# Kernel optimization log

Hardware: AMD Instinct MI355X
Metric: run time of the kernel (lower is better)

The kernel has to match this reference:

```python
import jax, jax.numpy as jnp
import numpy as np

N = 2000
E = 128
H = 8
DH = E // H
K = 32  # max_neighbors
CLAMP = 1e4


def _sanitize(t):
    t = jnp.nan_to_num(t, nan=0.0, posinf=CLAMP, neginf=-CLAMP)
    return jnp.clip(t, -CLAMP, CLAMP)


def _layernorm(h, g, b, eps=1e-5):
    mu = h.mean(-1, keepdims=True)
    var = ((h - mu) ** 2).mean(-1, keepdims=True)
    return (h - mu) * jax.lax.rsqrt(var + eps) * g + b


def setup_inputs() -> dict:
    key = jax.random.key(0)
    ks = jax.random.split(key, 8)
    x = jax.random.normal(ks[0], (N, E), dtype=jnp.float32)
    coords9 = jax.random.normal(ks[1], (N, 9), dtype=jnp.float32)
    prompt_signal = jax.random.normal(ks[2], (E,), dtype=jnp.float32)
    pe_w = jax.random.normal(ks[3], (3, 32), dtype=jnp.float32) / np.sqrt(3.0)
    pe_b = jnp.zeros((32,), jnp.float32)
    pe_g = jnp.ones((32,), jnp.float32)
    pe_bt = jnp.zeros((32,), jnp.float32)
    in_w = jax.random.normal(ks[4], (3 * E, E), dtype=jnp.float32) / np.sqrt(E)
    in_b = jnp.zeros((3 * E,), jnp.float32)
    out_w = jax.random.normal(ks[5], (E, E), dtype=jnp.float32) / np.sqrt(E)
    out_b = jnp.zeros((E,), jnp.float32)
    return {"x": x, "coords9": coords9, "prompt_signal": prompt_signal,
            "pe_w": pe_w, "pe_b": pe_b, "pe_g": pe_g, "pe_bt": pe_bt,
            "in_w": in_w, "in_b": in_b, "out_w": out_w, "out_b": out_b}


def reference(x, coords9, prompt_signal, pe_w, pe_b, pe_g, pe_bt, in_w, in_b, out_w, out_b):
    n = x.shape[0]
    verts = coords9.reshape(n, 3, 3)
    cent = verts.mean(axis=1)  # (N,3)

    # pairwise centroid distances (only geo-relation channel that affects the output;
    # cos_angles/area_ratios/boundary_sharing feed geo_bias which is dead code in forward)
    diff = cent[:, None, :] - cent[None, :, :]
    dist = jnp.sqrt(jnp.sum(diff * diff, axis=-1) + 1e-20)  # (N,N)

    # positional encoder: Linear(3,32) -> GELU(exact) -> LayerNorm(32)
    pe = jax.nn.gelu(cent @ pe_w + pe_b, approximate=False)
    pe = _layernorm(pe, pe_g, pe_bt)  # (N,32)

    prompt_enhanced = x + prompt_signal[None, :]
    pos_enhanced = jnp.concatenate([prompt_enhanced[:, : 3 * E // 4], pe], axis=-1)  # (N,128)

    # top-K nearest neighbors -> additive attention mask (0 for kept, -inf-like otherwise)
    _, topk_idx = jax.lax.top_k(-dist, K)  # (N,K) smallest distances
    big_neg = jnp.float32(-1e9)
    attn_mask = jnp.full((n, n), big_neg, dtype=jnp.float32)
    attn_mask = attn_mask.at[jnp.arange(n)[:, None], topk_idx].set(0.0)

    # nn.MultiheadAttention (self-attention, eval mode -> no dropout)
    qkv = pos_enhanced @ in_w.T + in_b  # (N,3E)
    q, k, v = jnp.split(qkv, 3, axis=-1)
    q = q.reshape(n, H, DH).transpose(1, 0, 2)  # (H,N,DH)
    k = k.reshape(n, H, DH).transpose(1, 0, 2)
    v = v.reshape(n, H, DH).transpose(1, 0, 2)
    scores = jnp.einsum('hnd,hmd->hnm', q, k) / np.sqrt(DH) + attn_mask[None]
    probs = jax.nn.softmax(scores, axis=-1)
    o = jnp.einsum('hnm,hmd->hnd', probs, v)  # (H,N,DH)
    o = o.transpose(1, 0, 2).reshape(n, E)
    out = o @ out_w.T + out_b
    return _sanitize(out)
```

## Files before the change

### kernel.cpp

```cpp
#include <hip/hip_runtime.h>
#include <math.h>

#define N_NODES 2000
#define E_DIM   128
#define QKV_W   384

__global__ __launch_bounds__(256) void prep_kernel(
    const float* __restrict__ x, const float* __restrict__ coords9,
    const float* __restrict__ ps, const float* __restrict__ pe_w,
    const float* __restrict__ pe_b, const float* __restrict__ pe_g,
    const float* __restrict__ pe_bt,
    float* __restrict__ cent, float* __restrict__ pos)
{
    int tid = threadIdx.x;
    int g = tid >> 5, lane = tid & 31;
    int row = blockIdx.x * 8 + g;

    const float* c9 = coords9 + row * 9;
    float cx = (c9[0] + c9[3] + c9[6]) * (1.0f / 3.0f);
    float cy = (c9[1] + c9[4] + c9[7]) * (1.0f / 3.0f);
    float cz = (c9[2] + c9[5] + c9[8]) * (1.0f / 3.0f);
    if (lane < 3) cent[row * 3 + lane] = (lane == 0) ? cx : ((lane == 1) ? cy : cz);

    #pragma unroll
    for (int k = 0; k < 3; ++k) {
        int c = lane + 32 * k;
        pos[row * E_DIM + c] = x[row * E_DIM + c] + ps[c];
    }

    int j = lane;
    float h = cx * pe_w[j] + cy * pe_w[32 + j] + cz * pe_w[64 + j] + pe_b[j];
    float ge = 0.5f * h * (1.0f + erff(h * 0.7071067811865476f));
    float s = ge;
    #pragma unroll
    for (int m = 16; m >= 1; m >>= 1) s += __shfl_xor(s, m);
    float mu = s * (1.0f / 32.0f);
    float d = ge - mu;
    float v = d * d;
    #pragma unroll
    for (int m = 16; m >= 1; m >>= 1) v += __shfl_xor(v, m);
    float var = v * (1.0f / 32.0f);
    float y = d * (1.0f / sqrtf(var + 1e-5f)) * pe_g[j] + pe_bt[j];
    pos[row * E_DIM + 96 + j] = y;
}

__global__ __launch_bounds__(256) void qkv_kernel(
    const float* __restrict__ pos, const float* __restrict__ in_w,
    const float* __restrict__ in_b, float* __restrict__ qkv)
{
    __shared__ __align__(16) float As[128 * 32];
    int tid = threadIdx.x;
    int rt = blockIdx.x / 3, ct = blockIdx.x % 3;
    int rbase = rt * 32, cbase = ct * 128;

    {
        int r = tid & 31, e0 = (tid >> 5) * 16;
        int row = rbase + r;
        #pragma unroll
        for (int q = 0; q < 4; ++q) {
            int e = e0 + q * 4;
            float4 vv = (row < N_NODES) ? *(const float4*)&pos[row * E_DIM + e]
                                        : make_float4(0.f, 0.f, 0.f, 0.f);
            As[(e + 0) * 32 + r] = vv.x;
            As[(e + 1) * 32 + r] = vv.y;
            As[(e + 2) * 32 + r] = vv.z;
            As[(e + 3) * 32 + r] = vv.w;
        }
    }
    __syncthreads();

    int cg = tid & 31, rg = tid >> 5;
    int c0 = cbase + cg * 4, r0 = rg * 4;
    float acc[4][4];
    #pragma unroll
    for (int i = 0; i < 4; ++i)
        #pragma unroll
        for (int jj = 0; jj < 4; ++jj) acc[i][jj] = 0.f;

    for (int k0 = 0; k0 < 128; k0 += 4) {
        float4 a0 = *(const float4*)&As[(k0 + 0) * 32 + r0];
        float4 a1 = *(const float4*)&As[(k0 + 1) * 32 + r0];
        float4 a2 = *(const float4*)&As[(k0 + 2) * 32 + r0];
        float4 a3 = *(const float4*)&As[(k0 + 3) * 32 + r0];
        #pragma unroll
        for (int ci = 0; ci < 4; ++ci) {
            float4 b = *(const float4*)&in_w[(c0 + ci) * E_DIM + k0];
            acc[0][ci] += a0.x * b.x + a1.x * b.y + a2.x * b.z + a3.x * b.w;
            acc[1][ci] += a0.y * b.x + a1.y * b.y + a2.y * b.z + a3.y * b.w;
            acc[2][ci] += a0.z * b.x + a1.z * b.y + a2.z * b.z + a3.z * b.w;
            acc[3][ci] += a0.w * b.x + a1.w * b.y + a2.w * b.z + a3.w * b.w;
        }
    }

    #pragma unroll
    for (int ri = 0; ri < 4; ++ri) {
        int row = rbase + r0 + ri;
        if (row < N_NODES) {
            float4 o4;
            o4.x = acc[ri][0] + in_b[c0 + 0];
            o4.y = acc[ri][1] + in_b[c0 + 1];
            o4.z = acc[ri][2] + in_b[c0 + 2];
            o4.w = acc[ri][3] + in_b[c0 + 3];
            *(float4*)&qkv[row * QKV_W + c0] = o4;
        }
    }
}

__global__ __launch_bounds__(256) void attn_kernel(
    const float* __restrict__ cent, const float* __restrict__ qkv,
    float* __restrict__ o_out)
{
    __shared__ unsigned int hist[256];
    __shared__ float wMin[4], wMax[4];
    __shared__ float sh_lo, sh_scale;
    __shared__ int sh_b, sh_nless, sh_sel, sh_eq;
    __shared__ int waveSum[4];
    __shared__ int topk[32];
    __shared__ int eqIdx[256];
    __shared__ unsigned int eqKey[256];
    __shared__ __align__(16) float qs[128];
    __shared__ float pr[256];

    int tid = threadIdx.x;
    int row = blockIdx.x;
    int lane = tid & 63, wid = tid >> 6;

    float cix = cent[row * 3 + 0], ciy = cent[row * 3 + 1], ciz = cent[row * 3 + 2];
    unsigned int kbits[8];
    bool valid[8];
    float lmin = __int_as_float(0x7f800000);
    float lmax = __int_as_float(0xff800000);
    {
        #pragma clang fp contract(off)
        #pragma unroll
        for (int l = 0; l < 8; ++l) {
            int j = tid + 256 * l;
            valid[l] = (j < N_NODES);
            float key = __int_as_float(0x7f800000);
            if (valid[l]) {
                float dx = cix - cent[j * 3 + 0];
                float dy = ciy - cent[j * 3 + 1];
                float dz = ciz - cent[j * 3 + 2];
                float a = dx * dx;
                float b = dy * dy;
                float c = dz * dz;
                float d2 = ((a + b) + c) + 1e-20f;
                key = sqrtf(d2);
                lmin = fminf(lmin, key);
                lmax = fmaxf(lmax, key);
            }
            kbits[l] = __float_as_uint(key);
        }
    }

    #pragma unroll
    for (int m = 32; m >= 1; m >>= 1) {
        lmin = fminf(lmin, __shfl_xor(lmin, m));
        lmax = fmaxf(lmax, __shfl_xor(lmax, m));
    }
    if (lane == 0) { wMin[wid] = lmin; wMax[wid] = lmax; }
    hist[tid] = 0u;
    if (tid == 0) { sh_sel = 0; sh_eq = 0; }
    __syncthreads();
    if (tid == 0) {
        float lo = fminf(fminf(wMin[0], wMin[1]), fminf(wMin[2], wMin[3]));
        float hi = fmaxf(fmaxf(wMax[0], wMax[1]), fmaxf(wMax[2], wMax[3]));
        sh_lo = lo;
        sh_scale = 255.0f / fmaxf(hi - lo, 1e-30f);
    }
    __syncthreads();
    float lo = sh_lo, scale = sh_scale;

    #pragma unroll
    for (int l = 0; l < 8; ++l) {
        if (valid[l]) {
            float key = __uint_as_float(kbits[l]);
            int bin = (int)((key - lo) * scale);
            bin = min(max(bin, 0), 255);
            atomicAdd(&hist[bin], 1u);
        }
    }
    __syncthreads();

    int h = (int)hist[tid];
    int incl = h;
    #pragma unroll
    for (int dd = 1; dd < 64; dd <<= 1) {
        int u = __shfl_up(incl, dd);
        if (lane >= dd) incl += u;
    }
    if (lane == 63) waveSum[wid] = incl;
    __syncthreads();
    int off = 0;
    for (int w = 0; w < wid; ++w) off += waveSum[w];
    int cum = incl + off;
    if (cum >= 32 && (cum - h) < 32) {
        sh_b = tid;
        sh_nless = cum - h;
    }
    __syncthreads();

    int b = sh_b;
    int req = 32 - sh_nless;

    #pragma unroll
    for (int l = 0; l < 8; ++l) {
        if (valid[l]) {
            float key = __uint_as_float(kbits[l]);
            int bin = (int)((key - lo) * scale);
            bin = min(max(bin, 0), 255);
            int j = tid + 256 * l;
            if (bin < b) {
                int p = atomicAdd(&sh_sel, 1);
                topk[p] = j;
            } else if (bin == b) {
                int e = atomicAdd(&sh_eq, 1);
                if (e < 256) { eqIdx[e] = j; eqKey[e] = kbits[l]; }
            }
        }
    }
    if (tid < 128) qs[tid] = qkv[row * QKV_W + tid];
    __syncthreads();

    int eq = min(sh_eq, 256);
    if (tid < eq) {
        int myIdx = eqIdx[tid];
        unsigned int myKey = eqKey[tid];
        int rank = 0;
        for (int u = 0; u < eq; ++u) {
            unsigned int ku = eqKey[u];
            rank += (ku < myKey || (ku == myKey && eqIdx[u] < myIdx)) ? 1 : 0;
        }
        if (rank < req) {
            int p = atomicAdd(&sh_sel, 1);
            topk[p] = myIdx;
        }
    }
    __syncthreads();

    {
        int hh = tid >> 5, j = tid & 31;
        int jj = topk[j];
        const float4* kp = (const float4*)&qkv[jj * QKV_W + 128 + hh * 16];
        const float4* qp = (const float4*)&qs[hh * 16];
        float s = 0.f;
        #pragma unroll
        for (int i = 0; i < 4; ++i) {
            float4 kv = kp[i], qv = qp[i];
            s += qv.x * kv.x + qv.y * kv.y + qv.z * kv.z + qv.w * kv.w;
        }
        s *= 0.25f;
        float m = s;
        #pragma unroll
        for (int msk = 16; msk >= 1; msk >>= 1) m = fmaxf(m, __shfl_xor(m, msk));
        float p = expf(s - m);
        float su = p;
        #pragma unroll
        for (int msk = 16; msk >= 1; msk >>= 1) su += __shfl_xor(su, msk);
        pr[tid] = p / su;
    }
    __syncthreads();

    if (tid < 128) {
        int hh = tid >> 4;
        float acc = 0.f;
        #pragma unroll
        for (int j = 0; j < 32; ++j) {
            int jj = topk[j];
            acc += pr[hh * 32 + j] * qkv[jj * QKV_W + 256 + tid];
        }
        o_out[row * E_DIM + tid] = acc;
    }
}

__device__ __forceinline__ float sanitize(float v)
{
    v = (v == v) ? v : 0.f;
    return fminf(fmaxf(v, -1e4f), 1e4f);
}

__global__ __launch_bounds__(256) void proj_kernel(
    const float* __restrict__ o_in, const float* __restrict__ out_w,
    const float* __restrict__ out_b, float* __restrict__ out)
{
    __shared__ __align__(16) float Os[128 * 16];
    int tid = threadIdx.x;
    int rbase = blockIdx.x * 16;

    {
        int r = tid & 15, e0 = (tid >> 4) * 8;
        #pragma unroll
        for (int q = 0; q < 2; ++q) {
            int e = e0 + q * 4;
            float4 vv = *(const float4*)&o_in[(rbase + r) * E_DIM + e];
            Os[(e + 0) * 16 + r] = vv.x;
            Os[(e + 1) * 16 + r] = vv.y;
            Os[(e + 2) * 16 + r] = vv.z;
            Os[(e + 3) * 16 + r] = vv.w;
        }
    }
    __syncthreads();

    int cg = tid & 31, rg = tid >> 5;
    int c0 = cg * 4, r0 = rg * 2;
    float acc[2][4];
    #pragma unroll
    for (int i = 0; i < 2; ++i)
        #pragma unroll
        for (int jj = 0; jj < 4; ++jj) acc[i][jj] = 0.f;

    for (int k0 = 0; k0 < 128; k0 += 4) {
        float2 a0 = *(const float2*)&Os[(k0 + 0) * 16 + r0];
        float2 a1 = *(const float2*)&Os[(k0 + 1) * 16 + r0];
        float2 a2 = *(const float2*)&Os[(k0 + 2) * 16 + r0];
        float2 a3 = *(const float2*)&Os[(k0 + 3) * 16 + r0];
        #pragma unroll
        for (int ci = 0; ci < 4; ++ci) {
            float4 b = *(const float4*)&out_w[(c0 + ci) * E_DIM + k0];
            acc[0][ci] += a0.x * b.x + a1.x * b.y + a2.x * b.z + a3.x * b.w;
            acc[1][ci] += a0.y * b.x + a1.y * b.y + a2.y * b.z + a3.y * b.w;
        }
    }

    #pragma unroll
    for (int ri = 0; ri < 2; ++ri) {
        int row = rbase + r0 + ri;
        float4 o4;
        o4.x = sanitize(acc[ri][0] + out_b[c0 + 0]);
        o4.y = sanitize(acc[ri][1] + out_b[c0 + 1]);
        o4.z = sanitize(acc[ri][2] + out_b[c0 + 2]);
        o4.w = sanitize(acc[ri][3] + out_b[c0 + 3]);
        *(float4*)&out[row * E_DIM + c0] = o4;
    }
}

extern "C" void kernel_launch(void* const* d_in, const int* in_sizes, int n_in,
                              void* d_out, int out_size, void* d_ws, size_t ws_size,
                              hipStream_t stream)
{
    const float* x      = (const float*)d_in[0];
    const float* coords = (const float*)d_in[1];
    const float* ps     = (const float*)d_in[2];
    const float* pe_w   = (const float*)d_in[3];
    const float* pe_b   = (const float*)d_in[4];
    const float* pe_g   = (const float*)d_in[5];
    const float* pe_bt  = (const float*)d_in[6];
    const float* in_w   = (const float*)d_in[7];
    const float* in_b   = (const float*)d_in[8];
    const float* out_w  = (const float*)d_in[9];
    const float* out_b  = (const float*)d_in[10];
    float* out = (float*)d_out;

    float* ws   = (float*)d_ws;
    float* cent = ws;
    float* pos  = ws + 6016;
    float* qkvb = ws + 6016 + 256000;
    float* ob   = ws + 6016 + 256000 + 768000;

    prep_kernel<<<250, 256, 0, stream>>>(x, coords, ps, pe_w, pe_b, pe_g, pe_bt, cent, pos);
    qkv_kernel<<<189, 256, 0, stream>>>(pos, in_w, in_b, qkvb);
    attn_kernel<<<2000, 256, 0, stream>>>(cent, qkvb, ob);
    proj_kernel<<<125, 256, 0, stream>>>(ob, out_w, out_b, out);
}
```

Before: 124.1 us.

## Fuse prep into QKV GEMM and output projection into attention kernel

Cuts the pipeline from four launches to two. The positional-encoding and prompt-add step now writes straight into the QKV GEMM's shared-memory tile, which is padded to reduce bank conflicts. The output projection runs per row inside the attention kernel as a 128x128 GEMV, and centroids are stored as separate x/y/z arrays for coalesced distance loads. This removes the intermediate pos and o buffers and two launches. In exchange, each of the 3 column tiles recomputes the prep work, and every attention block rereads out_w (64KB) from cache.

```diff
diff --git a/kernel.cpp b/kernel.cpp
--- a/kernel.cpp
+++ b/kernel.cpp
@@ -4,68 +4,58 @@
 #define N_NODES 2000
 #define E_DIM   128
 #define QKV_W   384
-
-__global__ __launch_bounds__(256) void prep_kernel(
+#define LDA     36
+
+__global__ __launch_bounds__(256) void prep_qkv_kernel(
     const float* __restrict__ x, const float* __restrict__ coords9,
     const float* __restrict__ ps, const float* __restrict__ pe_w,
     const float* __restrict__ pe_b, const float* __restrict__ pe_g,
-    const float* __restrict__ pe_bt,
-    float* __restrict__ cent, float* __restrict__ pos)
+    const float* __restrict__ pe_bt, const float* __restrict__ in_w,
+    const float* __restrict__ in_b,
+    float* __restrict__ cx_, float* __restrict__ cy_, float* __restrict__ cz_,
+    float* __restrict__ qkv)
 {
-    int tid = threadIdx.x;
-    int g = tid >> 5, lane = tid & 31;
-    int row = blockIdx.x * 8 + g;
-
-    const float* c9 = coords9 + row * 9;
-    float cx = (c9[0] + c9[3] + c9[6]) * (1.0f / 3.0f);
-    float cy = (c9[1] + c9[4] + c9[7]) * (1.0f / 3.0f);
-    float cz = (c9[2] + c9[5] + c9[8]) * (1.0f / 3.0f);
-    if (lane < 3) cent[row * 3 + lane] = (lane == 0) ? cx : ((lane == 1) ? cy : cz);
-
-    #pragma unroll
-    for (int k = 0; k < 3; ++k) {
-        int c = lane + 32 * k;
-        pos[row * E_DIM + c] = x[row * E_DIM + c] + ps[c];
-    }
-
-    int j = lane;
-    float h = cx * pe_w[j] + cy * pe_w[32 + j] + cz * pe_w[64 + j] + pe_b[j];
-    float ge = 0.5f * h * (1.0f + erff(h * 0.7071067811865476f));
-    float s = ge;
-    #pragma unroll
-    for (int m = 16; m >= 1; m >>= 1) s += __shfl_xor(s, m);
-    float mu = s * (1.0f / 32.0f);
-    float d = ge - mu;
-    float v = d * d;
-    #pragma unroll
-    for (int m = 16; m >= 1; m >>= 1) v += __shfl_xor(v, m);
-    float var = v * (1.0f / 32.0f);
-    float y = d * (1.0f / sqrtf(var + 1e-5f)) * pe_g[j] + pe_bt[j];
-    pos[row * E_DIM + 96 + j] = y;
-}
-
-__global__ __launch_bounds__(256) void qkv_kernel(
-    const float* __restrict__ pos, const float* __restrict__ in_w,
-    const float* __restrict__ in_b, float* __restrict__ qkv)
-{
-    __shared__ __align__(16) float As[128 * 32];
+    __shared__ __align__(16) float As[E_DIM * LDA];
     int tid = threadIdx.x;
     int rt = blockIdx.x / 3, ct = blockIdx.x % 3;
     int rbase = rt * 32, cbase = ct * 128;
-
-    {
-        int r = tid & 31, e0 = (tid >> 5) * 16;
-        int row = rbase + r;
-        #pragma unroll
-        for (int q = 0; q < 4; ++q) {
-            int e = e0 + q * 4;
-            float4 vv = (row < N_NODES) ? *(const float4*)&pos[row * E_DIM + e]
-                                        : make_float4(0.f, 0.f, 0.f, 0.f);
-            As[(e + 0) * 32 + r] = vv.x;
-            As[(e + 1) * 32 + r] = vv.y;
-            As[(e + 2) * 32 + r] = vv.z;
-            As[(e + 3) * 32 + r] = vv.w;
-        }
+    int g = tid >> 5, lane = tid & 31;
+
+    #pragma unroll
+    for (int rr = 0; rr < 4; ++rr) {
+        int rl = rr * 8 + g;
+        int row = rbase + rl;
+        bool vr = (row < N_NODES);
+        float cx = 0.f, cy = 0.f, cz = 0.f;
+        if (vr) {
+            const float* c9 = coords9 + row * 9;
+            cx = (c9[0] + c9[3] + c9[6]) * (1.0f / 3.0f);
+            cy = (c9[1] + c9[4] + c9[7]) * (1.0f / 3.0f);
+            cz = (c9[2] + c9[5] + c9[8]) * (1.0f / 3.0f);
+        }
+        if (ct == 0 && vr && lane == 0) { cx_[row] = cx; cy_[row] = cy; cz_[row] = cz; }
+
+        #pragma unroll
+        for (int k = 0; k < 3; ++k) {
+            int c = lane + 32 * k;
+            float v = vr ? (x[row * E_DIM + c] + ps[c]) : 0.f;
+            As[c * LDA + rl] = v;
+        }
+
+        int j = lane;
+        float h = cx * pe_w[j] + cy * pe_w[32 + j] + cz * pe_w[64 + j] + pe_b[j];
+        float ge = 0.5f * h * (1.0f + erff(h * 0.7071067811865476f));
+        float s = ge;
+        #pragma unroll
+        for (int m = 16; m >= 1; m >>= 1) s += __shfl_xor(s, m);
+        float mu = s * (1.0f / 32.0f);
+        float d = ge - mu;
+        float v2 = d * d;
+        #pragma unroll
+        for (int m = 16; m >= 1; m >>= 1) v2 += __shfl_xor(v2, m);
+        float var = v2 * (1.0f / 32.0f);
+        float y = d * (1.0f / sqrtf(var + 1e-5f)) * pe_g[j] + pe_bt[j];
+        As[(96 + j) * LDA + rl] = vr ? y : 0.f;
     }
     __syncthreads();
 
@@ -78,10 +68,10 @@
         for (int jj = 0; jj < 4; ++jj) acc[i][jj] = 0.f;
 
     for (int k0 = 0; k0 < 128; k0 += 4) {
-        float4 a0 = *(const float4*)&As[(k0 + 0) * 32 + r0];
-        float4 a1 = *(const float4*)&As[(k0 + 1) * 32 + r0];
-        float4 a2 = *(const float4*)&As[(k0 + 2) * 32 + r0];
-        float4 a3 = *(const float4*)&As[(k0 + 3) * 32 + r0];
+        float4 a0 = *(const float4*)&As[(k0 + 0) * LDA + r0];
+        float4 a1 = *(const float4*)&As[(k0 + 1) * LDA + r0];
+        float4 a2 = *(const float4*)&As[(k0 + 2) * LDA + r0];
+        float4 a3 = *(const float4*)&As[(k0 + 3) * LDA + r0];
         #pragma unroll
         for (int ci = 0; ci < 4; ++ci) {
             float4 b = *(const float4*)&in_w[(c0 + ci) * E_DIM + k0];
@@ -106,9 +96,17 @@
     }
 }
 
-__global__ __launch_bounds__(256) void attn_kernel(
-    const float* __restrict__ cent, const float* __restrict__ qkv,
-    float* __restrict__ o_out)
+__device__ __forceinline__ float sanitize(float v)
+{
+    v = (v == v) ? v : 0.f;
+    return fminf(fmaxf(v, -1e4f), 1e4f);
+}
+
+__global__ __launch_bounds__(256) void attn_proj_kernel(
+    const float* __restrict__ cx_, const float* __restrict__ cy_,
+    const float* __restrict__ cz_, const float* __restrict__ qkv,
+    const float* __restrict__ out_w, const float* __restrict__ out_b,
+    float* __restrict__ out)
 {
     __shared__ unsigned int hist[256];
     __shared__ float wMin[4], wMax[4];
@@ -120,12 +118,13 @@
     __shared__ unsigned int eqKey[256];
     __shared__ __align__(16) float qs[128];
     __shared__ float pr[256];
+    __shared__ __align__(16) float os[128];
 
     int tid = threadIdx.x;
     int row = blockIdx.x;
     int lane = tid & 63, wid = tid >> 6;
 
-    float cix = cent[row * 3 + 0], ciy = cent[row * 3 + 1], ciz = cent[row * 3 + 2];
+    float cix = cx_[row], ciy = cy_[row], ciz = cz_[row];
     unsigned int kbits[8];
     bool valid[8];
     float lmin = __int_as_float(0x7f800000);
@@ -138,9 +137,9 @@
             valid[l] = (j < N_NODES);
             float key = __int_as_float(0x7f800000);
             if (valid[l]) {
-                float dx = cix - cent[j * 3 + 0];
-                float dy = ciy - cent[j * 3 + 1];
-                float dz = ciz - cent[j * 3 + 2];
+                float dx = cix - cx_[j];
+                float dy = ciy - cy_[j];
+                float dz = ciz - cz_[j];
                 float a = dx * dx;
                 float b = dy * dy;
                 float c = dz * dz;
@@ -269,68 +268,20 @@
             int jj = topk[j];
             acc += pr[hh * 32 + j] * qkv[jj * QKV_W + 256 + tid];
         }
-        o_out[row * E_DIM + tid] = acc;
-    }
-}
-
-__device__ __forceinline__ float sanitize(float v)
-{
-    v = (v == v) ? v : 0.f;
-    return fminf(fmaxf(v, -1e4f), 1e4f);
-}
-
-__global__ __launch_bounds__(256) void proj_kernel(
-    const float* __restrict__ o_in, const float* __restrict__ out_w,
-    const float* __restrict__ out_b, float* __restrict__ out)
-{
-    __shared__ __align__(16) float Os[128 * 16];
-    int tid = threadIdx.x;
-    int rbase = blockIdx.x * 16;
-
-    {
-        int r = tid & 15, e0 = (tid >> 4) * 8;
-        #pragma unroll
-        for (int q = 0; q < 2; ++q) {
-            int e = e0 + q * 4;
-            float4 vv = *(const float4*)&o_in[(rbase + r) * E_DIM + e];
-            Os[(e + 0) * 16 + r] = vv.x;
-            Os[(e + 1) * 16 + r] = vv.y;
-            Os[(e + 2) * 16 + r] = vv.z;
-            Os[(e + 3) * 16 + r] = vv.w;
-        }
-    }
-    __syncthreads();
-
-    int cg = tid & 31, rg = tid >> 5;
-    int c0 = cg * 4, r0 = rg * 2;
-    float acc[2][4];
-    #pragma unroll
-    for (int i = 0; i < 2; ++i)
-        #pragma unroll
-        for (int jj = 0; jj < 4; ++jj) acc[i][jj] = 0.f;
-
-    for (int k0 = 0; k0 < 128; k0 += 4) {
-        float2 a0 = *(const float2*)&Os[(k0 + 0) * 16 + r0];
-        float2 a1 = *(const float2*)&Os[(k0 + 1) * 16 + r0];
-        float2 a2 = *(const float2*)&Os[(k0 + 2) * 16 + r0];
-        float2 a3 = *(const float2*)&Os[(k0 + 3) * 16 + r0];
-        #pragma unroll
-        for (int ci = 0; ci < 4; ++ci) {
-            float4 b = *(const float4*)&out_w[(c0 + ci) * E_DIM + k0];
-            acc[0][ci] += a0.x * b.x + a1.x * b.y + a2.x * b.z + a3.x * b.w;
-            acc[1][ci] += a0.y * b.x + a1.y * b.y + a2.y * b.z + a3.y * b.w;
-        }
-    }
-
-    #pragma unroll
-    for (int ri = 0; ri < 2; ++ri) {
-        int row = rbase + r0 + ri;
-        float4 o4;
-        o4.x = sanitize(acc[ri][0] + out_b[c0 + 0]);
-        o4.y = sanitize(acc[ri][1] + out_b[c0 + 1]);
-        o4.z = sanitize(acc[ri][2] + out_b[c0 + 2]);
-        o4.w = sanitize(acc[ri][3] + out_b[c0 + 3]);
-        *(float4*)&out[row * E_DIM + c0] = o4;
+        os[tid] = acc;
+    }
+    __syncthreads();
+
+    if (tid < 128) {
+        const float* wr = out_w + tid * E_DIM;
+        float a = 0.f;
+        #pragma unroll
+        for (int e = 0; e < 128; e += 4) {
+            float4 w4 = *(const float4*)&wr[e];
+            float4 o4 = *(const float4*)&os[e];
+            a += o4.x * w4.x + o4.y * w4.y + o4.z * w4.z + o4.w * w4.w;
+        }
+        out[row * E_DIM + tid] = sanitize(a + out_b[tid]);
     }
 }
 
@@ -351,14 +302,13 @@
     const float* out_b  = (const float*)d_in[10];
     float* out = (float*)d_out;
 
-    float* ws   = (float*)d_ws;
-    float* cent = ws;
-    float* pos  = ws + 6016;
-    float* qkvb = ws + 6016 + 256000;
-    float* ob   = ws + 6016 + 256000 + 768000;
-
-    prep_kernel<<<250, 256, 0, stream>>>(x, coords, ps, pe_w, pe_b, pe_g, pe_bt, cent, pos);
-    qkv_kernel<<<189, 256, 0, stream>>>(pos, in_w, in_b, qkvb);
-    attn_kernel<<<2000, 256, 0, stream>>>(cent, qkvb, ob);
-    proj_kernel<<<125, 256, 0, stream>>>(ob, out_w, out_b, out);
+    float* ws  = (float*)d_ws;
+    float* cxp = ws;
+    float* cyp = ws + 2048;
+    float* czp = ws + 4096;
+    float* qkvb = ws + 6144;
+
+    prep_qkv_kernel<<<189, 256, 0, stream>>>(x, coords, ps, pe_w, pe_b, pe_g, pe_bt,
+                                             in_w, in_b, cxp, cyp, czp, qkvb);
+    attn_proj_kernel<<<2000, 256, 0, stream>>>(cxp, cyp, czp, qkvb, out_w, out_b, out);
 }
```

New measurement: 123.8 us. About the same (-0.3%).
